# Performance work log

Measured on AMD Instinct MI355X. Metric: run time of the kernel, lower is better.

The kernel has to match this reference:

```python
import jax, jax.numpy as jnp
import numpy as np

B, L, C, K, S = 8, 4096, 512, 5, 8


def setup_inputs() -> dict:
    key = jax.random.key(0)
    ks = jax.random.split(key, 5)
    x = jax.random.normal(ks[0], (B, L, C), dtype=jnp.float32)
    # contiguous random partition of [0, L) into S segments per batch row
    rng = np.random.default_rng(0)
    cuts = np.sort(rng.integers(1, L, size=(B, S - 1)), axis=1)
    starts = np.concatenate([np.zeros((B, 1), np.int64), cuts.astype(np.int64)], axis=1)
    ends = np.concatenate([cuts.astype(np.int64), np.full((B, 1), L, np.int64)], axis=1)
    segment_boundaries = jnp.asarray(np.stack([starts, ends], axis=-1))  # [B,S,2]
    fan = 1.0 / np.sqrt(K)
    w_dw = jax.random.normal(ks[1], (C, K), dtype=jnp.float32) * fan
    b_dw = jax.random.normal(ks[2], (C,), dtype=jnp.float32) * 0.01
    w_pw = jax.random.normal(ks[3], (C, C), dtype=jnp.float32) * (1.0 / np.sqrt(C))
    b_pw = jax.random.normal(ks[4], (C,), dtype=jnp.float32) * 0.01
    return {"x": x, "segment_boundaries": segment_boundaries,
            "w_dw": w_dw, "b_dw": b_dw, "w_pw": w_pw, "b_pw": b_pw}


def reference(x, segment_boundaries, w_dw, b_dw, w_pw, b_pw):
    # x: [B,L,C]; segment_boundaries: [B,S,2]; w_dw: [C,K]; w_pw: [C_out,C_in]
    Bx, Lx, Cx = x.shape
    Kx = w_dw.shape[1]
    starts = segment_boundaries[..., 0]  # [B,S]
    ends = segment_boundaries[..., 1]    # [B,S]
    pos = jnp.arange(Lx)
    in_seg = (pos[None, None, :] >= starts[..., None]) & (pos[None, None, :] < ends[..., None])  # [B,S,L]
    covered = in_seg.any(axis=1)                                  # [B,L]
    seg_id = jnp.where(covered, jnp.argmax(in_seg, axis=1), -1)   # [B,L]

    # causal depthwise conv with left zero-pad per segment (no cross-segment leakage)
    acc = jnp.zeros_like(x)
    for d in range(Kx):  # d = how far back we look; tap index = K-1-d
        if d == 0:
            x_s, id_s = x, seg_id
        else:
            x_s = jnp.pad(x, ((0, 0), (d, 0), (0, 0)))[:, :Lx]
            id_s = jnp.pad(seg_id, ((0, 0), (d, 0)), constant_values=-2)[:, :Lx]
        m = ((seg_id == id_s) & covered).astype(x.dtype)          # [B,L]
        acc = acc + w_dw[:, Kx - 1 - d] * x_s * m[..., None]
    dw = acc + b_dw                                               # [B,L,C]
    pw = jnp.einsum('blc,dc->bld', dw, w_pw) + b_pw               # pointwise 1x1 conv
    return pw * covered[..., None].astype(x.dtype)                # zeros outside segments
```

## Files before the change

kernel.cpp:

```cpp
#include <hip/hip_runtime.h>
#include <hip/hip_bf16.h>
#include <climits>

typedef __bf16 bf16;
typedef __bf16 bf16x4 __attribute__((ext_vector_type(4)));
typedef __bf16 bf16x8 __attribute__((ext_vector_type(8)));
typedef float f32x4 __attribute__((ext_vector_type(4)));

#define NB 8
#define L_ 4096
#define C_ 512
#define KW 5
#define NS 8
#define BM 64

__global__ __launch_bounds__(256) void bias_kernel(
    const float* __restrict__ w_pw, const float* __restrict__ b_dw,
    const float* __restrict__ b_pw, float* __restrict__ bias2) {
  const int n = blockIdx.x;
  const int t = threadIdx.x;
  float2 v = *(const float2*)(w_pw + n * C_ + 2 * t);
  float2 bb = *(const float2*)(b_dw + 2 * t);
  float s = v.x * bb.x + v.y * bb.y;
#pragma unroll
  for (int off = 32; off; off >>= 1) s += __shfl_down(s, off, 64);
  __shared__ float part[4];
  if ((t & 63) == 0) part[t >> 6] = s;
  __syncthreads();
  if (t == 0) bias2[n] = b_pw[n] + part[0] + part[1] + part[2] + part[3];
}

__global__ __launch_bounds__(256) void pack_kernel(const float* __restrict__ w_pw,
                                                   bf16* __restrict__ pk) {
  const int gid = blockIdx.x * 256 + threadIdx.x;
  const int lane = gid & 63;
  const int nf = (gid >> 6) & 3;
  const int wnn = (gid >> 8) & 7;
  const int kk = gid >> 11;
  const int n = wnn * 64 + nf * 16 + (lane & 15);
  const int c = kk * 32 + (lane >> 4) * 8;
  const float* s = w_pw + n * C_ + c;
  float4 a = *(const float4*)s;
  float4 b4 = *(const float4*)(s + 4);
  bf16x8 h;
  h[0] = (bf16)a.x; h[1] = (bf16)a.y; h[2] = (bf16)a.z; h[3] = (bf16)a.w;
  h[4] = (bf16)b4.x; h[5] = (bf16)b4.y; h[6] = (bf16)b4.z; h[7] = (bf16)b4.w;
  *(bf16x8*)(pk + (size_t)gid * 8) = h;
}

__global__ __launch_bounds__(512, 4) void fused_kernel(
    const float* __restrict__ x, const int* __restrict__ segb,
    const float* __restrict__ w_dw, const bf16* __restrict__ pk,
    const float* __restrict__ bias2, float* __restrict__ out) {
  __shared__ __align__(16) bf16 As[BM * C_];

  const int t = threadIdx.x;
  const int lane = t & 63;
  const int b = blockIdx.x >> 6;
  const int l0 = (blockIdx.x & 63) << 6;

  const int q = t & 127;
  const int r0 = (t >> 7) << 4;

  float4 raw[5];
#pragma unroll
  for (int i = 0; i < 5; ++i)
    raw[i] = *(const float4*)(w_dw + q * 20 + i * 4);
  f32x4 wt[5];
#pragma unroll
  for (int m = 0; m < 5; ++m)
#pragma unroll
    for (int i = 0; i < 4; ++i) {
      const int f = i * 5 + m;
      wt[m][i] = ((const float*)&raw[f >> 2])[f & 3];
    }

  const int* sb = segb + b * NS * 2;
  int stv[NS];
#pragma unroll
  for (int s = 0; s < NS; ++s) stv[s] = sb[2 * s];
  auto nxt = [&](int l) {
    int nn = INT_MAX;
#pragma unroll
    for (int s = 0; s < NS; ++s)
      nn = (stv[s] > l && stv[s] < nn) ? stv[s] : nn;
    return nn;
  };
  int ns = nxt(l0 + r0 - 4);

  const float* gxb = x + (size_t)(b * L_ + l0 + r0) * C_ + q * 4;

  const f32x4 z4 = (f32x4){0.f, 0.f, 0.f, 0.f};
  f32x4 w0 = z4, w1 = z4, w2 = z4, w3 = z4;

#pragma unroll
  for (int i = 0; i < 4; ++i) {
    const int l = l0 + r0 - 4 + i;
    f32x4 nv = z4;
    if (l >= 0) nv = *(const f32x4*)(gxb + (ptrdiff_t)(i - 4) * C_);
    if (l == ns) { w0 = z4; w1 = z4; w2 = z4; w3 = z4; ns = nxt(l); }
    w0 = w1; w1 = w2; w2 = w3; w3 = nv;
  }

  auto dorow = [&](int l, f32x4& A, f32x4& B4, f32x4& Cc, f32x4& D,
                   const f32x4& E, int rloc) {
    if (l == ns) { A = z4; B4 = z4; Cc = z4; D = z4; ns = nxt(l); }
    f32x4 r;
#pragma unroll
    for (int i = 0; i < 4; ++i) {
      float a = A[i] * wt[0][i];
      a = fmaf(B4[i], wt[1][i], a);
      a = fmaf(Cc[i], wt[2][i], a);
      a = fmaf(D[i], wt[3][i], a);
      a = fmaf(E[i], wt[4][i], a);
      r[i] = a;
    }
    bf16x4 h;
#pragma unroll
    for (int i = 0; i < 4; ++i) h[i] = (bf16)r[i];
    const int u = q ^ ((rloc & 7) << 1);
    *(bf16x4*)&As[rloc * 512 + u * 4] = h;
  };

#pragma unroll
  for (int g = 0; g < 4; ++g) {
    const int lb = l0 + r0 + g * 4;
    f32x4 n0 = *(const f32x4*)(gxb + (ptrdiff_t)(g * 4 + 0) * C_);
    f32x4 n1 = *(const f32x4*)(gxb + (ptrdiff_t)(g * 4 + 1) * C_);
    f32x4 n2 = *(const f32x4*)(gxb + (ptrdiff_t)(g * 4 + 2) * C_);
    f32x4 n3 = *(const f32x4*)(gxb + (ptrdiff_t)(g * 4 + 3) * C_);
    dorow(lb + 0, w0, w1, w2, w3, n0, r0 + g * 4 + 0);
    dorow(lb + 1, w1, w2, w3, n0, n1, r0 + g * 4 + 1);
    dorow(lb + 2, w2, w3, n0, n1, n2, r0 + g * 4 + 2);
    dorow(lb + 3, w3, n0, n1, n2, n3, r0 + g * 4 + 3);
    w0 = n0; w1 = n1; w2 = n2; w3 = n3;
  }

  __syncthreads();

  const int wn = t >> 6;
  const int cg = lane >> 4;
  const int rx = lane & 7;

  int aRow[4];
#pragma unroll
  for (int mf = 0; mf < 4; ++mf) aRow[mf] = (mf * 16 + (lane & 15)) * 512;
  const bf16* pw = pk + wn * 2048 + lane * 8;

  f32x4 acc[4][4];
#pragma unroll
  for (int i = 0; i < 4; ++i)
#pragma unroll
    for (int j = 0; j < 4; ++j) acc[i][j] = z4;

#pragma unroll 1
  for (int kk = 0; kk < 16; ++kk) {
    const bf16* pws = pw + kk * 16384;
    bf16x8 bb[4];
#pragma unroll
    for (int nf = 0; nf < 4; ++nf)
      bb[nf] = *(const bf16x8*)(pws + nf * 512);
    const int ao = ((kk * 4 + cg) ^ rx) << 3;
    bf16x8 af[4];
#pragma unroll
    for (int mf = 0; mf < 4; ++mf)
      af[mf] = *(const bf16x8*)&As[aRow[mf] + ao];
    __builtin_amdgcn_s_setprio(1);
#pragma unroll
    for (int nf = 0; nf < 4; ++nf)
#pragma unroll
      for (int mf = 0; mf < 4; ++mf)
        acc[mf][nf] = __builtin_amdgcn_mfma_f32_16x16x32_bf16(
            af[mf], bb[nf], acc[mf][nf], 0, 0, 0);
    __builtin_amdgcn_s_setprio(0);
  }

  const int col0 = wn * 64 + (lane & 15);
  float bia[4];
#pragma unroll
  for (int nf = 0; nf < 4; ++nf) bia[nf] = bias2[col0 + nf * 16];
  const int rb0 = l0 + (cg << 2);
#pragma unroll
  for (int mf = 0; mf < 4; ++mf) {
#pragma unroll
    for (int i = 0; i < 4; ++i) {
      const int row = rb0 + mf * 16 + i;
      float* o = out + (size_t)(b * L_ + row) * C_ + col0;
#pragma unroll
      for (int nf = 0; nf < 4; ++nf) o[nf * 16] = acc[mf][nf][i] + bia[nf];
    }
  }
}

extern "C" void kernel_launch(void* const* d_in, const int* in_sizes, int n_in,
                              void* d_out, int out_size, void* d_ws,
                              size_t ws_size, hipStream_t stream) {
  const float* x = (const float*)d_in[0];
  const int* segb = (const int*)d_in[1];
  const float* w_dw = (const float*)d_in[2];
  const float* b_dw = (const float*)d_in[3];
  const float* w_pw = (const float*)d_in[4];
  const float* b_pw = (const float*)d_in[5];
  float* out = (float*)d_out;

  float* bias2 = (float*)d_ws;
  bf16* pk = (bf16*)((char*)d_ws + 4096);

  bias_kernel<<<C_, 256, 0, stream>>>(w_pw, b_dw, b_pw, bias2);
  pack_kernel<<<128, 256, 0, stream>>>(w_pw, pk);
  fused_kernel<<<NB * L_ / BM, 512, 0, stream>>>(x, segb, w_dw, pk, bias2,
                                                 out);
}
```

Baseline: 42.39 us.

## Split fused conv+GEMM into separate conv and MFMA-packed GEMM kernels

Unfuses the depthwise conv from the pointwise GEMM. A new conv kernel writes bf16 activations into global memory already laid out in MFMA fragment order. A new GEMM kernel uses 1024-thread blocks and loads that tile straight into LDS with global_load_lds, then runs a double-buffered K loop over 16 waves, each owning 32 output columns. This aims to raise occupancy and overlap LDS and global loads with MFMA. In exchange it adds an extra global write and read of the bf16 intermediate (about 32MB of traffic) and one more kernel launch.

```diff
diff --git a/kernel.cpp b/kernel.cpp
--- a/kernel.cpp
+++ b/kernel.cpp
@@ -12,7 +12,11 @@
 #define C_ 512
 #define KW 5
 #define NS 8
-#define BM 64
+
+#define GLOAD_LDS16(g, l)                                                      \
+  __builtin_amdgcn_global_load_lds(                                            \
+      (const __attribute__((address_space(1))) void*)(g),                      \
+      (__attribute__((address_space(3))) void*)(l), 16, 0, 0)
 
 __global__ __launch_bounds__(256) void bias_kernel(
     const float* __restrict__ w_pw, const float* __restrict__ b_dw,
@@ -30,14 +34,14 @@
   if (t == 0) bias2[n] = b_pw[n] + part[0] + part[1] + part[2] + part[3];
 }
 
-__global__ __launch_bounds__(256) void pack_kernel(const float* __restrict__ w_pw,
-                                                   bf16* __restrict__ pk) {
+__global__ __launch_bounds__(256) void packB_kernel(
+    const float* __restrict__ w_pw, bf16* __restrict__ pkB) {
   const int gid = blockIdx.x * 256 + threadIdx.x;
   const int lane = gid & 63;
-  const int nf = (gid >> 6) & 3;
-  const int wnn = (gid >> 8) & 7;
+  const int nf = (gid >> 6) & 1;
+  const int wv = (gid >> 7) & 15;
   const int kk = gid >> 11;
-  const int n = wnn * 64 + nf * 16 + (lane & 15);
+  const int n = wv * 32 + nf * 16 + (lane & 15);
   const int c = kk * 32 + (lane >> 4) * 8;
   const float* s = w_pw + n * C_ + c;
   float4 a = *(const float4*)s;
@@ -45,22 +49,18 @@
   bf16x8 h;
   h[0] = (bf16)a.x; h[1] = (bf16)a.y; h[2] = (bf16)a.z; h[3] = (bf16)a.w;
   h[4] = (bf16)b4.x; h[5] = (bf16)b4.y; h[6] = (bf16)b4.z; h[7] = (bf16)b4.w;
-  *(bf16x8*)(pk + (size_t)gid * 8) = h;
-}
-
-__global__ __launch_bounds__(512, 4) void fused_kernel(
+  *(bf16x8*)(pkB + (size_t)gid * 8) = h;
+}
+
+__global__ __launch_bounds__(256) void conv_kernel(
     const float* __restrict__ x, const int* __restrict__ segb,
-    const float* __restrict__ w_dw, const bf16* __restrict__ pk,
-    const float* __restrict__ bias2, float* __restrict__ out) {
-  __shared__ __align__(16) bf16 As[BM * C_];
-
-  const int t = threadIdx.x;
-  const int lane = t & 63;
-  const int b = blockIdx.x >> 6;
-  const int l0 = (blockIdx.x & 63) << 6;
-
-  const int q = t & 127;
-  const int r0 = (t >> 7) << 4;
+    const float* __restrict__ w_dw, bf16* __restrict__ dwp) {
+  const int g = blockIdx.x * 256 + threadIdx.x;
+  const int q = g & 127;
+  const int rest = g >> 7;
+  const int b = rest >> 7;
+  const int chunk = rest & 127;
+  const int l0 = chunk << 5;
 
   float4 raw[5];
 #pragma unroll
@@ -86,24 +86,26 @@
       nn = (stv[s] > l && stv[s] < nn) ? stv[s] : nn;
     return nn;
   };
-  int ns = nxt(l0 + r0 - 4);
-
-  const float* gxb = x + (size_t)(b * L_ + l0 + r0) * C_ + q * 4;
+  int ns = nxt(l0 - 4);
+
+  const float* xbase = x + ((size_t)(b * L_ + l0)) * C_ + q * 4;
+  bf16* dbase = dwp + (size_t)b * 2097152 + (q >> 3) * 512 +
+                ((q >> 1) & 3) * 128 + (q & 1) * 4;
 
   const f32x4 z4 = (f32x4){0.f, 0.f, 0.f, 0.f};
   f32x4 w0 = z4, w1 = z4, w2 = z4, w3 = z4;
 
 #pragma unroll
   for (int i = 0; i < 4; ++i) {
-    const int l = l0 + r0 - 4 + i;
+    const int l = l0 - 4 + i;
     f32x4 nv = z4;
-    if (l >= 0) nv = *(const f32x4*)(gxb + (ptrdiff_t)(i - 4) * C_);
+    if (l >= 0) nv = *(const f32x4*)(xbase + (ptrdiff_t)(i - 4) * C_);
     if (l == ns) { w0 = z4; w1 = z4; w2 = z4; w3 = z4; ns = nxt(l); }
     w0 = w1; w1 = w2; w2 = w3; w3 = nv;
   }
 
   auto dorow = [&](int l, f32x4& A, f32x4& B4, f32x4& Cc, f32x4& D,
-                   const f32x4& E, int rloc) {
+                   const f32x4& E) {
     if (l == ns) { A = z4; B4 = z4; Cc = z4; D = z4; ns = nxt(l); }
     f32x4 r;
 #pragma unroll
@@ -118,67 +120,101 @@
     bf16x4 h;
 #pragma unroll
     for (int i = 0; i < 4; ++i) h[i] = (bf16)r[i];
-    const int u = q ^ ((rloc & 7) << 1);
-    *(bf16x4*)&As[rloc * 512 + u * 4] = h;
+    *(bf16x4*)(dbase + (l >> 4) * 8192 + (l & 15) * 8) = h;
   };
 
-#pragma unroll
-  for (int g = 0; g < 4; ++g) {
-    const int lb = l0 + r0 + g * 4;
-    f32x4 n0 = *(const f32x4*)(gxb + (ptrdiff_t)(g * 4 + 0) * C_);
-    f32x4 n1 = *(const f32x4*)(gxb + (ptrdiff_t)(g * 4 + 1) * C_);
-    f32x4 n2 = *(const f32x4*)(gxb + (ptrdiff_t)(g * 4 + 2) * C_);
-    f32x4 n3 = *(const f32x4*)(gxb + (ptrdiff_t)(g * 4 + 3) * C_);
-    dorow(lb + 0, w0, w1, w2, w3, n0, r0 + g * 4 + 0);
-    dorow(lb + 1, w1, w2, w3, n0, n1, r0 + g * 4 + 1);
-    dorow(lb + 2, w2, w3, n0, n1, n2, r0 + g * 4 + 2);
-    dorow(lb + 3, w3, n0, n1, n2, n3, r0 + g * 4 + 3);
+#pragma unroll 1
+  for (int g8 = 0; g8 < 8; ++g8) {
+    const int lb = l0 + g8 * 4;
+    f32x4 n0 = *(const f32x4*)(xbase + (ptrdiff_t)(g8 * 4 + 0) * C_);
+    f32x4 n1 = *(const f32x4*)(xbase + (ptrdiff_t)(g8 * 4 + 1) * C_);
+    f32x4 n2 = *(const f32x4*)(xbase + (ptrdiff_t)(g8 * 4 + 2) * C_);
+    f32x4 n3 = *(const f32x4*)(xbase + (ptrdiff_t)(g8 * 4 + 3) * C_);
+    dorow(lb + 0, w0, w1, w2, w3, n0);
+    dorow(lb + 1, w1, w2, w3, n0, n1);
+    dorow(lb + 2, w2, w3, n0, n1, n2);
+    dorow(lb + 3, w3, n0, n1, n2, n3);
     w0 = n0; w1 = n1; w2 = n2; w3 = n3;
   }
+}
+
+__global__ __launch_bounds__(1024) void gemm_kernel(
+    const bf16* __restrict__ dwp, const bf16* __restrict__ pkB,
+    const float* __restrict__ bias2, float* __restrict__ out) {
+  __shared__ __align__(16) bf16 As[32768];
+
+  const int t = threadIdx.x;
+  const int lane = t & 63;
+  const int wv = t >> 6;
+  const int b = blockIdx.x >> 6;
+  const int mt = blockIdx.x & 63;
+  const int l0 = mt << 6;
+
+  const bf16* asrc = dwp + ((size_t)b * 256 + mt * 4) * 8192;
+#pragma unroll
+  for (int i = 0; i < 4; ++i)
+    GLOAD_LDS16(asrc + (i * 1024 + t) * 8, As + (i * 1024 + (t & ~63)) * 8);
+
+  const bf16* pb = pkB + ((size_t)wv * 2 * 64 + lane) * 8;
+
+  bf16x8 bbA[2], bbB[2], afA[4], afB[4];
+#pragma unroll
+  for (int nf = 0; nf < 2; ++nf)
+    bbA[nf] = *(const bf16x8*)(pb + nf * 512);
 
   __syncthreads();
 
-  const int wn = t >> 6;
-  const int cg = lane >> 4;
-  const int rx = lane & 7;
-
-  int aRow[4];
-#pragma unroll
-  for (int mf = 0; mf < 4; ++mf) aRow[mf] = (mf * 16 + (lane & 15)) * 512;
-  const bf16* pw = pk + wn * 2048 + lane * 8;
-
-  f32x4 acc[4][4];
+  const int aL = lane * 8;
+#pragma unroll
+  for (int mf = 0; mf < 4; ++mf)
+    afA[mf] = *(const bf16x8*)&As[mf * 16 * 64 * 8 + aL];
+
+  f32x4 acc[4][2];
 #pragma unroll
   for (int i = 0; i < 4; ++i)
 #pragma unroll
-    for (int j = 0; j < 4; ++j) acc[i][j] = z4;
+    for (int j = 0; j < 2; ++j) acc[i][j] = (f32x4){0.f, 0.f, 0.f, 0.f};
 
 #pragma unroll 1
-  for (int kk = 0; kk < 16; ++kk) {
-    const bf16* pws = pw + kk * 16384;
-    bf16x8 bb[4];
-#pragma unroll
-    for (int nf = 0; nf < 4; ++nf)
-      bb[nf] = *(const bf16x8*)(pws + nf * 512);
-    const int ao = ((kk * 4 + cg) ^ rx) << 3;
-    bf16x8 af[4];
+  for (int k2 = 0; k2 < 16; k2 += 2) {
+#pragma unroll
+    for (int nf = 0; nf < 2; ++nf)
+      bbB[nf] = *(const bf16x8*)(pb + (k2 + 1) * 16384 + nf * 512);
 #pragma unroll
     for (int mf = 0; mf < 4; ++mf)
-      af[mf] = *(const bf16x8*)&As[aRow[mf] + ao];
+      afB[mf] = *(const bf16x8*)&As[(mf * 16 + (k2 + 1)) * 512 + aL];
     __builtin_amdgcn_s_setprio(1);
 #pragma unroll
-    for (int nf = 0; nf < 4; ++nf)
+    for (int nf = 0; nf < 2; ++nf)
 #pragma unroll
       for (int mf = 0; mf < 4; ++mf)
         acc[mf][nf] = __builtin_amdgcn_mfma_f32_16x16x32_bf16(
-            af[mf], bb[nf], acc[mf][nf], 0, 0, 0);
+            afA[mf], bbA[nf], acc[mf][nf], 0, 0, 0);
     __builtin_amdgcn_s_setprio(0);
-  }
-
-  const int col0 = wn * 64 + (lane & 15);
-  float bia[4];
-#pragma unroll
-  for (int nf = 0; nf < 4; ++nf) bia[nf] = bias2[col0 + nf * 16];
+
+    if (k2 + 2 < 16) {
+#pragma unroll
+      for (int nf = 0; nf < 2; ++nf)
+        bbA[nf] = *(const bf16x8*)(pb + (k2 + 2) * 16384 + nf * 512);
+#pragma unroll
+      for (int mf = 0; mf < 4; ++mf)
+        afA[mf] = *(const bf16x8*)&As[(mf * 16 + (k2 + 2)) * 512 + aL];
+    }
+    __builtin_amdgcn_s_setprio(1);
+#pragma unroll
+    for (int nf = 0; nf < 2; ++nf)
+#pragma unroll
+      for (int mf = 0; mf < 4; ++mf)
+        acc[mf][nf] = __builtin_amdgcn_mfma_f32_16x16x32_bf16(
+            afB[mf], bbB[nf], acc[mf][nf], 0, 0, 0);
+    __builtin_amdgcn_s_setprio(0);
+  }
+
+  const int col0 = wv * 32 + (lane & 15);
+  const int cg = lane >> 4;
+  float bia[2];
+#pragma unroll
+  for (int nf = 0; nf < 2; ++nf) bia[nf] = bias2[col0 + nf * 16];
   const int rb0 = l0 + (cg << 2);
 #pragma unroll
   for (int mf = 0; mf < 4; ++mf) {
@@ -187,7 +223,7 @@
       const int row = rb0 + mf * 16 + i;
       float* o = out + (size_t)(b * L_ + row) * C_ + col0;
 #pragma unroll
-      for (int nf = 0; nf < 4; ++nf) o[nf * 16] = acc[mf][nf][i] + bia[nf];
+      for (int nf = 0; nf < 2; ++nf) o[nf * 16] = acc[mf][nf][i] + bia[nf];
     }
   }
 }
@@ -204,10 +240,11 @@
   float* out = (float*)d_out;
 
   float* bias2 = (float*)d_ws;
-  bf16* pk = (bf16*)((char*)d_ws + 4096);
+  bf16* pkB = (bf16*)((char*)d_ws + 4096);
+  bf16* dwp = (bf16*)((char*)d_ws + (1 << 20));
 
   bias_kernel<<<C_, 256, 0, stream>>>(w_pw, b_dw, b_pw, bias2);
-  pack_kernel<<<128, 256, 0, stream>>>(w_pw, pk);
-  fused_kernel<<<NB * L_ / BM, 512, 0, stream>>>(x, segb, w_dw, pk, bias2,
-                                                 out);
-}
+  packB_kernel<<<128, 256, 0, stream>>>(w_pw, pkB);
+  conv_kernel<<<512, 256, 0, stream>>>(x, segb, w_dw, dwp);
+  gemm_kernel<<<NB * L_ / 64, 1024, 0, stream>>>(dwp, pkB, bias2, out);
+}
```

Result: slower. 63.08 us (+48.8%).

## Warp-specialize fused kernel into producer and MFMA consumer waves over two tiles

Applied to the files above, without the earlier changes.

The block grows to 1024 threads and handles two 64-row tiles. Eight producer waves compute the depthwise conv into double-buffered LDS, while eight consumer waves run the pointwise MFMA GEMM and register-prefetch B fragments across k-steps. The aim is to overlap the global loads and VALU conv of tile 1 with the GEMM of tile 0. In exchange it doubles LDS use (128KB per block), halves the grid, and adds barrier coupling between the wave groups. The barrier pairing looks consistent: each side issues two barriers.

```diff
diff --git a/kernel.cpp b/kernel.cpp
--- a/kernel.cpp
+++ b/kernel.cpp
@@ -13,6 +13,18 @@
 #define KW 5
 #define NS 8
 #define BM 64
+
+#define BARRIER_MEM                                                            \
+  do {                                                                         \
+    __builtin_amdgcn_sched_barrier(0);                                         \
+    __builtin_amdgcn_s_barrier();                                              \
+    __builtin_amdgcn_sched_barrier(0);                                         \
+  } while (0)
+#define DSFLUSH_BARRIER                                                        \
+  do {                                                                         \
+    asm volatile("s_waitcnt lgkmcnt(0)" ::: "memory");                         \
+    BARRIER_MEM;                                                               \
+  } while (0)
 
 __global__ __launch_bounds__(256) void bias_kernel(
     const float* __restrict__ w_pw, const float* __restrict__ b_dw,
@@ -48,146 +60,187 @@
   *(bf16x8*)(pk + (size_t)gid * 8) = h;
 }
 
-__global__ __launch_bounds__(512, 4) void fused_kernel(
+__global__ __launch_bounds__(1024, 4) void fused_kernel(
     const float* __restrict__ x, const int* __restrict__ segb,
-    const float* __restrict__ w_dw, const bf16* __restrict__ pk,
+    const float* __restrict__ w_dw, const bf16* __restrict__ pkB,
     const float* __restrict__ bias2, float* __restrict__ out) {
-  __shared__ __align__(16) bf16 As[BM * C_];
+  __shared__ __align__(16) bf16 As[2][BM * C_];
 
   const int t = threadIdx.x;
   const int lane = t & 63;
-  const int b = blockIdx.x >> 6;
-  const int l0 = (blockIdx.x & 63) << 6;
-
-  const int q = t & 127;
-  const int r0 = (t >> 7) << 4;
-
-  float4 raw[5];
-#pragma unroll
-  for (int i = 0; i < 5; ++i)
-    raw[i] = *(const float4*)(w_dw + q * 20 + i * 4);
-  f32x4 wt[5];
-#pragma unroll
-  for (int m = 0; m < 5; ++m)
-#pragma unroll
-    for (int i = 0; i < 4; ++i) {
-      const int f = i * 5 + m;
-      wt[m][i] = ((const float*)&raw[f >> 2])[f & 3];
+  const int wid = t >> 6;
+  const int b = blockIdx.x >> 5;
+  const int base = (blockIdx.x & 31) << 7;
+
+  const f32x4 z4 = (f32x4){0.f, 0.f, 0.f, 0.f};
+
+  if (wid >= 8) {
+    const int t2 = t - 512;
+    const int q = t2 & 127;
+    const int r0 = (t2 >> 7) << 4;
+
+    float4 raw[5];
+#pragma unroll
+    for (int i = 0; i < 5; ++i)
+      raw[i] = *(const float4*)(w_dw + q * 20 + i * 4);
+    f32x4 wt[5];
+#pragma unroll
+    for (int m = 0; m < 5; ++m)
+#pragma unroll
+      for (int i = 0; i < 4; ++i) {
+        const int f = i * 5 + m;
+        wt[m][i] = ((const float*)&raw[f >> 2])[f & 3];
+      }
+
+    const int* sb = segb + b * NS * 2;
+    int stv[NS];
+#pragma unroll
+    for (int s = 0; s < NS; ++s) stv[s] = sb[2 * s];
+    auto nxt = [&](int l) {
+      int nn = INT_MAX;
+#pragma unroll
+      for (int s = 0; s < NS; ++s)
+        nn = (stv[s] > l && stv[s] < nn) ? stv[s] : nn;
+      return nn;
+    };
+
+#pragma unroll 1
+    for (int tile = 0; tile < 2; ++tile) {
+      const int l0 = base + (tile << 6);
+      bf16* Ab = (bf16*)As[tile];
+      int ns = nxt(l0 + r0 - 4);
+      const float* gxb = x + (size_t)(b * L_ + l0 + r0) * C_ + q * 4;
+
+      f32x4 w0 = z4, w1 = z4, w2 = z4, w3 = z4;
+#pragma unroll
+      for (int i = 0; i < 4; ++i) {
+        const int l = l0 + r0 - 4 + i;
+        f32x4 nv = z4;
+        if (l >= 0) nv = *(const f32x4*)(gxb + (ptrdiff_t)(i - 4) * C_);
+        if (l == ns) { w0 = z4; w1 = z4; w2 = z4; w3 = z4; ns = nxt(l); }
+        w0 = w1; w1 = w2; w2 = w3; w3 = nv;
+      }
+
+      auto dorow = [&](int l, f32x4& A, f32x4& B4, f32x4& Cc, f32x4& D,
+                       const f32x4& E, int rloc) {
+        if (l == ns) { A = z4; B4 = z4; Cc = z4; D = z4; ns = nxt(l); }
+        f32x4 r;
+#pragma unroll
+        for (int i = 0; i < 4; ++i) {
+          float a = A[i] * wt[0][i];
+          a = fmaf(B4[i], wt[1][i], a);
+          a = fmaf(Cc[i], wt[2][i], a);
+          a = fmaf(D[i], wt[3][i], a);
+          a = fmaf(E[i], wt[4][i], a);
+          r[i] = a;
+        }
+        bf16x4 h;
+#pragma unroll
+        for (int i = 0; i < 4; ++i) h[i] = (bf16)r[i];
+        const int u = q ^ ((rloc & 7) << 1);
+        *(bf16x4*)&Ab[rloc * 512 + u * 4] = h;
+      };
+
+#pragma unroll
+      for (int g = 0; g < 4; ++g) {
+        const int lb = l0 + r0 + g * 4;
+        f32x4 n0 = *(const f32x4*)(gxb + (ptrdiff_t)(g * 4 + 0) * C_);
+        f32x4 n1 = *(const f32x4*)(gxb + (ptrdiff_t)(g * 4 + 1) * C_);
+        f32x4 n2 = *(const f32x4*)(gxb + (ptrdiff_t)(g * 4 + 2) * C_);
+        f32x4 n3 = *(const f32x4*)(gxb + (ptrdiff_t)(g * 4 + 3) * C_);
+        dorow(lb + 0, w0, w1, w2, w3, n0, r0 + g * 4 + 0);
+        dorow(lb + 1, w1, w2, w3, n0, n1, r0 + g * 4 + 1);
+        dorow(lb + 2, w2, w3, n0, n1, n2, r0 + g * 4 + 2);
+        dorow(lb + 3, w3, n0, n1, n2, n3, r0 + g * 4 + 3);
+        w0 = n0; w1 = n1; w2 = n2; w3 = n3;
+      }
+      DSFLUSH_BARRIER;
     }
-
-  const int* sb = segb + b * NS * 2;
-  int stv[NS];
-#pragma unroll
-  for (int s = 0; s < NS; ++s) stv[s] = sb[2 * s];
-  auto nxt = [&](int l) {
-    int nn = INT_MAX;
-#pragma unroll
-    for (int s = 0; s < NS; ++s)
-      nn = (stv[s] > l && stv[s] < nn) ? stv[s] : nn;
-    return nn;
-  };
-  int ns = nxt(l0 + r0 - 4);
-
-  const float* gxb = x + (size_t)(b * L_ + l0 + r0) * C_ + q * 4;
-
-  const f32x4 z4 = (f32x4){0.f, 0.f, 0.f, 0.f};
-  f32x4 w0 = z4, w1 = z4, w2 = z4, w3 = z4;
-
-#pragma unroll
-  for (int i = 0; i < 4; ++i) {
-    const int l = l0 + r0 - 4 + i;
-    f32x4 nv = z4;
-    if (l >= 0) nv = *(const f32x4*)(gxb + (ptrdiff_t)(i - 4) * C_);
-    if (l == ns) { w0 = z4; w1 = z4; w2 = z4; w3 = z4; ns = nxt(l); }
-    w0 = w1; w1 = w2; w2 = w3; w3 = nv;
-  }
-
-  auto dorow = [&](int l, f32x4& A, f32x4& B4, f32x4& Cc, f32x4& D,
-                   const f32x4& E, int rloc) {
-    if (l == ns) { A = z4; B4 = z4; Cc = z4; D = z4; ns = nxt(l); }
-    f32x4 r;
-#pragma unroll
-    for (int i = 0; i < 4; ++i) {
-      float a = A[i] * wt[0][i];
-      a = fmaf(B4[i], wt[1][i], a);
-      a = fmaf(Cc[i], wt[2][i], a);
-      a = fmaf(D[i], wt[3][i], a);
-      a = fmaf(E[i], wt[4][i], a);
-      r[i] = a;
-    }
-    bf16x4 h;
-#pragma unroll
-    for (int i = 0; i < 4; ++i) h[i] = (bf16)r[i];
-    const int u = q ^ ((rloc & 7) << 1);
-    *(bf16x4*)&As[rloc * 512 + u * 4] = h;
-  };
-
-#pragma unroll
-  for (int g = 0; g < 4; ++g) {
-    const int lb = l0 + r0 + g * 4;
-    f32x4 n0 = *(const f32x4*)(gxb + (ptrdiff_t)(g * 4 + 0) * C_);
-    f32x4 n1 = *(const f32x4*)(gxb + (ptrdiff_t)(g * 4 + 1) * C_);
-    f32x4 n2 = *(const f32x4*)(gxb + (ptrdiff_t)(g * 4 + 2) * C_);
-    f32x4 n3 = *(const f32x4*)(gxb + (ptrdiff_t)(g * 4 + 3) * C_);
-    dorow(lb + 0, w0, w1, w2, w3, n0, r0 + g * 4 + 0);
-    dorow(lb + 1, w1, w2, w3, n0, n1, r0 + g * 4 + 1);
-    dorow(lb + 2, w2, w3, n0, n1, n2, r0 + g * 4 + 2);
-    dorow(lb + 3, w3, n0, n1, n2, n3, r0 + g * 4 + 3);
-    w0 = n0; w1 = n1; w2 = n2; w3 = n3;
-  }
-
-  __syncthreads();
-
-  const int wn = t >> 6;
-  const int cg = lane >> 4;
-  const int rx = lane & 7;
-
-  int aRow[4];
-#pragma unroll
-  for (int mf = 0; mf < 4; ++mf) aRow[mf] = (mf * 16 + (lane & 15)) * 512;
-  const bf16* pw = pk + wn * 2048 + lane * 8;
-
-  f32x4 acc[4][4];
-#pragma unroll
-  for (int i = 0; i < 4; ++i)
-#pragma unroll
-    for (int j = 0; j < 4; ++j) acc[i][j] = z4;
+  } else {
+    const int wn = wid;
+    const int cg = lane >> 4;
+    const int rx = lane & 7;
+
+    int aRow[4];
+#pragma unroll
+    for (int mf = 0; mf < 4; ++mf) aRow[mf] = (mf * 16 + (lane & 15)) * 512;
+    const bf16* pb = pkB + (size_t)wn * 2048 + lane * 8;
+
+    const int col0 = wn * 64 + (lane & 15);
+    float bia[4];
+#pragma unroll
+    for (int nf = 0; nf < 4; ++nf) bia[nf] = bias2[col0 + nf * 16];
+
+    bf16x8 bbA[4], bbB[4], af[4];
+#pragma unroll
+    for (int nf = 0; nf < 4; ++nf)
+      bbA[nf] = *(const bf16x8*)(pb + nf * 512);
 
 #pragma unroll 1
-  for (int kk = 0; kk < 16; ++kk) {
-    const bf16* pws = pw + kk * 16384;
-    bf16x8 bb[4];
-#pragma unroll
-    for (int nf = 0; nf < 4; ++nf)
-      bb[nf] = *(const bf16x8*)(pws + nf * 512);
-    const int ao = ((kk * 4 + cg) ^ rx) << 3;
-    bf16x8 af[4];
-#pragma unroll
-    for (int mf = 0; mf < 4; ++mf)
-      af[mf] = *(const bf16x8*)&As[aRow[mf] + ao];
-    __builtin_amdgcn_s_setprio(1);
-#pragma unroll
-    for (int nf = 0; nf < 4; ++nf)
-#pragma unroll
-      for (int mf = 0; mf < 4; ++mf)
-        acc[mf][nf] = __builtin_amdgcn_mfma_f32_16x16x32_bf16(
-            af[mf], bb[nf], acc[mf][nf], 0, 0, 0);
-    __builtin_amdgcn_s_setprio(0);
-  }
-
-  const int col0 = wn * 64 + (lane & 15);
-  float bia[4];
-#pragma unroll
-  for (int nf = 0; nf < 4; ++nf) bia[nf] = bias2[col0 + nf * 16];
-  const int rb0 = l0 + (cg << 2);
-#pragma unroll
-  for (int mf = 0; mf < 4; ++mf) {
-#pragma unroll
-    for (int i = 0; i < 4; ++i) {
-      const int row = rb0 + mf * 16 + i;
-      float* o = out + (size_t)(b * L_ + row) * C_ + col0;
-#pragma unroll
-      for (int nf = 0; nf < 4; ++nf) o[nf * 16] = acc[mf][nf][i] + bia[nf];
+    for (int tile = 0; tile < 2; ++tile) {
+      BARRIER_MEM;
+      const bf16* Ab = (const bf16*)As[tile];
+
+      f32x4 acc[4][4];
+#pragma unroll
+      for (int i = 0; i < 4; ++i)
+#pragma unroll
+        for (int j = 0; j < 4; ++j) acc[i][j] = z4;
+
+#pragma unroll 1
+      for (int kk = 0; kk < 16; kk += 2) {
+#pragma unroll
+        for (int nf = 0; nf < 4; ++nf)
+          bbB[nf] = *(const bf16x8*)(pb + (kk + 1) * 16384 + nf * 512);
+        const int ao = ((kk * 4 + cg) ^ rx) << 3;
+#pragma unroll
+        for (int mf = 0; mf < 4; ++mf)
+          af[mf] = *(const bf16x8*)&Ab[aRow[mf] + ao];
+        __builtin_amdgcn_s_setprio(1);
+#pragma unroll
+        for (int nf = 0; nf < 4; ++nf)
+#pragma unroll
+          for (int mf = 0; mf < 4; ++mf)
+            acc[mf][nf] = __builtin_amdgcn_mfma_f32_16x16x32_bf16(
+                af[mf], bbA[nf], acc[mf][nf], 0, 0, 0);
+        __builtin_amdgcn_s_setprio(0);
+
+        if (kk + 2 < 16) {
+#pragma unroll
+          for (int nf = 0; nf < 4; ++nf)
+            bbA[nf] = *(const bf16x8*)(pb + (kk + 2) * 16384 + nf * 512);
+        }
+        const int ao2 = (((kk + 1) * 4 + cg) ^ rx) << 3;
+#pragma unroll
+        for (int mf = 0; mf < 4; ++mf)
+          af[mf] = *(const bf16x8*)&Ab[aRow[mf] + ao2];
+        __builtin_amdgcn_s_setprio(1);
+#pragma unroll
+        for (int nf = 0; nf < 4; ++nf)
+#pragma unroll
+          for (int mf = 0; mf < 4; ++mf)
+            acc[mf][nf] = __builtin_amdgcn_mfma_f32_16x16x32_bf16(
+                af[mf], bbB[nf], acc[mf][nf], 0, 0, 0);
+        __builtin_amdgcn_s_setprio(0);
+      }
+
+      const int l0 = base + (tile << 6);
+      const int rb0 = l0 + (cg << 2);
+#pragma unroll
+      for (int mf = 0; mf < 4; ++mf) {
+#pragma unroll
+        for (int i = 0; i < 4; ++i) {
+          const int row = rb0 + mf * 16 + i;
+          float* o = out + (size_t)(b * L_ + row) * C_ + col0;
+#pragma unroll
+          for (int nf = 0; nf < 4; ++nf) o[nf * 16] = acc[mf][nf][i] + bia[nf];
+        }
+      }
+      if (tile == 0) {
+#pragma unroll
+        for (int nf = 0; nf < 4; ++nf)
+          bbA[nf] = *(const bf16x8*)(pb + nf * 512);
+      }
     }
   }
 }
@@ -204,10 +257,10 @@
   float* out = (float*)d_out;
 
   float* bias2 = (float*)d_ws;
-  bf16* pk = (bf16*)((char*)d_ws + 4096);
+  bf16* pkB = (bf16*)((char*)d_ws + 4096);
 
   bias_kernel<<<C_, 256, 0, stream>>>(w_pw, b_dw, b_pw, bias2);
-  pack_kernel<<<128, 256, 0, stream>>>(w_pw, pk);
-  fused_kernel<<<NB * L_ / BM, 512, 0, stream>>>(x, segb, w_dw, pk, bias2,
-                                                 out);
-}
+  pack_kernel<<<128, 256, 0, stream>>>(w_pw, pkB);
+  fused_kernel<<<NB * L_ / 128, 1024, 0, stream>>>(x, segb, w_dw, pkB, bias2,
+                                                   out);
+}
```

Measured after the change: 46.22 us. +9.0%, slower.

## Halve row tile to 32 and double-buffer pointwise weight fragments in registers

Applied to the files above, without the earlier changes.

Shrinks the per-block row tile from 64 to 32, which doubles the grid and halves the MFMA accumulator set per wave. The B-fragment loads of the packed weights are software-pipelined with two register buffers so the next k-step's loads overlap the current MFMAs. The LDS array is padded beyond what the tile needs, which looks aimed at capping blocks per CU. In exchange, the whole packed weight matrix is now read from cache by twice as many blocks, which raises L2 traffic.

```diff
diff --git a/kernel.cpp b/kernel.cpp
--- a/kernel.cpp
+++ b/kernel.cpp
@@ -12,7 +12,8 @@
 #define C_ 512
 #define KW 5
 #define NS 8
-#define BM 64
+#define BM 32
+#define AS_ELEMS (BM * C_ + 12288)
 
 __global__ __launch_bounds__(256) void bias_kernel(
     const float* __restrict__ w_pw, const float* __restrict__ b_dw,
@@ -52,15 +53,15 @@
     const float* __restrict__ x, const int* __restrict__ segb,
     const float* __restrict__ w_dw, const bf16* __restrict__ pk,
     const float* __restrict__ bias2, float* __restrict__ out) {
-  __shared__ __align__(16) bf16 As[BM * C_];
+  __shared__ __align__(16) bf16 As[AS_ELEMS];
 
   const int t = threadIdx.x;
   const int lane = t & 63;
-  const int b = blockIdx.x >> 6;
-  const int l0 = (blockIdx.x & 63) << 6;
+  const int b = blockIdx.x >> 7;
+  const int l0 = (blockIdx.x & 127) << 5;
 
   const int q = t & 127;
-  const int r0 = (t >> 7) << 4;
+  const int r0 = (t >> 7) << 3;
 
   float4 raw[5];
 #pragma unroll
@@ -123,7 +124,7 @@
   };
 
 #pragma unroll
-  for (int g = 0; g < 4; ++g) {
+  for (int g = 0; g < 2; ++g) {
     const int lb = l0 + r0 + g * 4;
     f32x4 n0 = *(const f32x4*)(gxb + (ptrdiff_t)(g * 4 + 0) * C_);
     f32x4 n1 = *(const f32x4*)(gxb + (ptrdiff_t)(g * 4 + 1) * C_);
@@ -142,36 +143,55 @@
   const int cg = lane >> 4;
   const int rx = lane & 7;
 
-  int aRow[4];
-#pragma unroll
-  for (int mf = 0; mf < 4; ++mf) aRow[mf] = (mf * 16 + (lane & 15)) * 512;
-  const bf16* pw = pk + wn * 2048 + lane * 8;
-
-  f32x4 acc[4][4];
-#pragma unroll
-  for (int i = 0; i < 4; ++i)
+  const int aRow0 = (lane & 15) * 512;
+  const int aRow1 = (16 + (lane & 15)) * 512;
+  const bf16* pb = pk + (size_t)wn * 2048 + lane * 8;
+
+  f32x4 acc[2][4];
+#pragma unroll
+  for (int i = 0; i < 2; ++i)
 #pragma unroll
     for (int j = 0; j < 4; ++j) acc[i][j] = z4;
 
+  bf16x8 bbA[4], bbB[4];
+#pragma unroll
+  for (int nf = 0; nf < 4; ++nf)
+    bbA[nf] = *(const bf16x8*)(pb + nf * 512);
+
 #pragma unroll 1
-  for (int kk = 0; kk < 16; ++kk) {
-    const bf16* pws = pw + kk * 16384;
-    bf16x8 bb[4];
+  for (int kk = 0; kk < 16; kk += 2) {
 #pragma unroll
     for (int nf = 0; nf < 4; ++nf)
-      bb[nf] = *(const bf16x8*)(pws + nf * 512);
+      bbB[nf] = *(const bf16x8*)(pb + (kk + 1) * 16384 + nf * 512);
     const int ao = ((kk * 4 + cg) ^ rx) << 3;
-    bf16x8 af[4];
-#pragma unroll
-    for (int mf = 0; mf < 4; ++mf)
-      af[mf] = *(const bf16x8*)&As[aRow[mf] + ao];
+    bf16x8 a0 = *(const bf16x8*)&As[aRow0 + ao];
+    bf16x8 a1 = *(const bf16x8*)&As[aRow1 + ao];
     __builtin_amdgcn_s_setprio(1);
 #pragma unroll
-    for (int nf = 0; nf < 4; ++nf)
-#pragma unroll
-      for (int mf = 0; mf < 4; ++mf)
-        acc[mf][nf] = __builtin_amdgcn_mfma_f32_16x16x32_bf16(
-            af[mf], bb[nf], acc[mf][nf], 0, 0, 0);
+    for (int nf = 0; nf < 4; ++nf) {
+      acc[0][nf] = __builtin_amdgcn_mfma_f32_16x16x32_bf16(a0, bbA[nf],
+                                                           acc[0][nf], 0, 0, 0);
+      acc[1][nf] = __builtin_amdgcn_mfma_f32_16x16x32_bf16(a1, bbA[nf],
+                                                           acc[1][nf], 0, 0, 0);
+    }
+    __builtin_amdgcn_s_setprio(0);
+
+    if (kk + 2 < 16) {
+#pragma unroll
+      for (int nf = 0; nf < 4; ++nf)
+        bbA[nf] = *(const bf16x8*)(pb + (kk + 2) * 16384 + nf * 512);
+    }
+    const int ao2 = (((kk + 1) * 4 + cg) ^ rx) << 3;
+    bf16x8 a2 = *(const bf16x8*)&As[aRow0 + ao2];
+    bf16x8 a3 = *(const bf16x8*)&As[aRow1 + ao2];
+    __builtin_amdgcn_s_setprio(1);
+#pragma unroll
+    for (int nf = 0; nf < 4; ++nf) {
+      acc[0][nf] = __builtin_amdgcn_mfma_f32_16x16x32_bf16(a2, bbB[nf],
+                                                           acc[0][nf], 0, 0, 0);
+      acc[1][nf] = __builtin_amdgcn_mfma_f32_16x16x32_bf16(a3, bbB[nf],
+                                                           acc[1][nf], 0, 0, 0);
+    }
     __builtin_amdgcn_s_setprio(0);
   }
 
@@ -181,7 +201,7 @@
   for (int nf = 0; nf < 4; ++nf) bia[nf] = bias2[col0 + nf * 16];
   const int rb0 = l0 + (cg << 2);
 #pragma unroll
-  for (int mf = 0; mf < 4; ++mf) {
+  for (int mf = 0; mf < 2; ++mf) {
 #pragma unroll
     for (int i = 0; i < 4; ++i) {
       const int row = rb0 + mf * 16 + i;
```

New measurement: 46.40 us. 9.5% more time.
